# Performance work log

Measured on AMD Instinct MI355X. Metric: run time of the kernel, lower is better.

## Reference

```python
import jax, jax.numpy as jnp
import numpy as np

NUM_HEADS = 16
HEAD_DIM = 32  # out_ch 512 / 16 heads

def _c(x):
    # last axis holds (real, imag) -> complex64
    return jax.lax.complex(x[..., 0], x[..., 1])

def setup_inputs() -> dict:
    key = jax.random.key(0)
    ks = jax.random.split(key, 9)
    B, S, C = 1, 2048, 512
    mk = lambda k, shp: jax.random.normal(k, shp, dtype=jnp.float32)
    return {
        "Q": mk(ks[0], (B, S, C, 2)),
        "V": mk(ks[1], (B, S, C, 2)),
        "K": mk(ks[2], (B, S, C, 2)),
        "Wq": mk(ks[3], (C, C, 2)) * (1.0 / np.sqrt(C)),
        "bq": mk(ks[4], (C, 2)) * 0.02,
        "Wk": mk(ks[5], (C, C, 2)) * (1.0 / np.sqrt(C)),
        "bk": mk(ks[6], (C, 2)) * 0.02,
        "Wv": mk(ks[7], (C, C, 2)) * (1.0 / np.sqrt(C)),
        "bv": mk(ks[8], (C, 2)) * 0.02,
    }

def _split_heads(x):
    B, S, D = x.shape
    return x.reshape(B, S, NUM_HEADS, HEAD_DIM).transpose(0, 2, 1, 3)  # [B,H,S,d]

def reference(Q, V, K, Wq, bq, Wk, bk, Wv, bv):
    Qc, Kc, Vc = _c(Q), _c(K), _c(V)
    # torch Linear: y = x @ W^T + b, W is [out, in]
    proj = lambda x, W, b: jnp.einsum('bsi,oi->bso', x, _c(W)) + _c(b)
    q = _split_heads(proj(Qc, Wq, bq))  # [B,H,S,d] complex64
    k = _split_heads(proj(Kc, Wk, bk))
    v = _split_heads(proj(Vc, Wv, bv))
    scores = jnp.einsum('bhqd,bhkd->bhqk', q, jnp.conj(k)) / np.sqrt(HEAD_DIM).astype(np.float32)
    weights = jax.nn.softmax(jnp.abs(scores), axis=-1)  # real [B,H,S,S]
    out = jnp.einsum('bhqk,bhkd->bhqd', weights.astype(v.dtype), v)  # complex
    B, H, S, d = out.shape
    out = out.transpose(0, 2, 1, 3).reshape(B, S, H * d)  # [B,S,out_ch]
    return jnp.stack([out.real, out.imag], axis=-1)  # [B,S,out_ch,2] float32
```

## Files before the change

kernel.cpp:

```cpp
#include <hip/hip_runtime.h>
#include <hip/hip_bf16.h>
#include <math.h>

#define S_LEN 2048
#define C_DIM 512
#define NH 16
#define HD 32
#define PLANE_U (NH * S_LEN * HD)
#define XF_OFF  (6*(size_t)PLANE_U)
#define WF_OFF  (12*(size_t)PLANE_U)
#define WPLF 262144

typedef __attribute__((ext_vector_type(8)))  short bf16x8;
typedef __attribute__((ext_vector_type(4)))  float f32x4;
typedef __attribute__((ext_vector_type(16))) float f32x16;
typedef __attribute__((ext_vector_type(4)))  unsigned int u32x4;

#if __has_builtin(__builtin_amdgcn_exp2f)
#define EXP2(x) __builtin_amdgcn_exp2f(x)
#else
#define EXP2(x) exp2f(x)
#endif

__device__ __forceinline__ unsigned int pk_bf16(float a, float b) {
    float2 f; f.x = a; f.y = b;
    __hip_bfloat162 t = __float22bfloat162_rn(f);
    return *reinterpret_cast<unsigned int*>(&t);
}

__global__ __launch_bounds__(256)
void xwcvt(const float* __restrict__ Q, const float* __restrict__ K,
           const float* __restrict__ V,
           const float* __restrict__ Wq, const float* __restrict__ Wk,
           const float* __restrict__ Wv, unsigned short* __restrict__ ws)
{
    if (blockIdx.x < 1536) {
        const int tid  = blockIdx.x*256 + threadIdx.x;
        const int z    = tid >> 17;
        const int rem  = tid & 131071;
        const int kidx = rem >> 11;
        const int s    = rem & 2047;
        const int k    = kidx * 8;
        const float2* x2 = (const float2*)(z == 0 ? Q : (z == 1 ? K : V));
        const float4* s4 = (const float4*)(x2 + (size_t)s*C_DIM + k);
        float4 f0 = s4[0], f1 = s4[1], f2v = s4[2], f3 = s4[3];
        u32x4 rh, ih;
        rh[0] = pk_bf16(f0.x, f0.z); rh[1] = pk_bf16(f1.x, f1.z);
        rh[2] = pk_bf16(f2v.x, f2v.z); rh[3] = pk_bf16(f3.x, f3.z);
        ih[0] = pk_bf16(f0.y, f0.w); ih[1] = pk_bf16(f1.y, f1.w);
        ih[2] = pk_bf16(f2v.y, f2v.w); ih[3] = pk_bf16(f3.y, f3.w);
        const int sb = s >> 4, lr = s & 15, g = kidx & 3, kc = kidx >> 2;
        const size_t off = ((size_t)(sb*16 + kc)*64 + g*16 + lr)*8;
        unsigned short* base = ws + XF_OFF + (size_t)z*2*PLANE_U;
        *(u32x4*)&base[off]           = rh;
        *(u32x4*)&base[PLANE_U + off] = ih;
    } else {
        const int tid  = (blockIdx.x - 1536)*256 + threadIdx.x;
        const int z    = tid >> 15;
        const int rem  = tid & 32767;
        const int kidx = rem >> 9;
        const int o    = rem & 511;
        const int k    = kidx * 8;
        const float2* w2 = (const float2*)(z == 0 ? Wq : (z == 1 ? Wk : Wv));
        const float4* s4 = (const float4*)(w2 + (size_t)o*C_DIM + k);
        float4 f0 = s4[0], f1 = s4[1], f2v = s4[2], f3 = s4[3];
        u32x4 rh, ih;
        rh[0] = pk_bf16(f0.x, f0.z); rh[1] = pk_bf16(f1.x, f1.z);
        rh[2] = pk_bf16(f2v.x, f2v.z); rh[3] = pk_bf16(f3.x, f3.z);
        ih[0] = pk_bf16(f0.y, f0.w); ih[1] = pk_bf16(f1.y, f1.w);
        ih[2] = pk_bf16(f2v.y, f2v.w); ih[3] = pk_bf16(f3.y, f3.w);
        const int ob = o >> 4, lr = o & 15, g = kidx & 3, kc = kidx >> 2;
        const size_t off = ((size_t)(ob*16 + kc)*64 + g*16 + lr)*8;
        unsigned short* base = ws + WF_OFF + (size_t)z*2*WPLF;
        *(u32x4*)&base[off]        = rh;
        *(u32x4*)&base[WPLF + off] = ih;
    }
}

__global__ __launch_bounds__(256)
void proj_mfma(const float* __restrict__ bq, const float* __restrict__ bk,
               const float* __restrict__ bv,
               unsigned short* __restrict__ ws)
{
    const int z = blockIdx.z;
    const float* b = (z == 0) ? bq : (z == 1 ? bk : bv);

    const int s0 = blockIdx.x * 32;
    const int o0 = blockIdx.y * 64;

    const unsigned short* xfR = ws + XF_OFF + (size_t)z*2*PLANE_U;
    const unsigned short* xfI = xfR + PLANE_U;
    const unsigned short* wfR = ws + WF_OFF + (size_t)z*2*WPLF;
    const unsigned short* wfI = wfR + WPLF;

    const int t    = threadIdx.x;
    const int wave = t >> 6;
    const int lane = t & 63;
    const int lr   = t & 15;
    const int g    = (t & 63) >> 4;

    const int ob = (o0 >> 4) + wave;
    const int sb = s0 >> 4;

    const f32x4 zf = {0.f,0.f,0.f,0.f};
    f32x4 accR[2], accI[2];
    #pragma unroll
    for (int i = 0; i < 2; ++i) { accR[i] = zf; accI[i] = zf; }

    size_t aoff = ((size_t)(ob*16)*64 + lane)*8;
    bf16x8 aRH = *(const bf16x8*)&wfR[aoff];
    bf16x8 aIH = *(const bf16x8*)&wfI[aoff];

    #pragma unroll
    for (int kc = 0; kc < 16; ++kc) {
        bf16x8 aIHn;
        #pragma unroll
        for (int j = 0; j < 4; ++j)
            ((unsigned int*)&aIHn)[j] = ((const unsigned int*)&aIH)[j] ^ 0x80008000u;

        const size_t b0 = ((size_t)(sb*16 + kc)*64 + lane)*8;
        const size_t b1 = ((size_t)((sb+1)*16 + kc)*64 + lane)*8;
        bf16x8 bRH0 = *(const bf16x8*)&xfR[b0];
        bf16x8 bIH0 = *(const bf16x8*)&xfI[b0];
        bf16x8 bRH1 = *(const bf16x8*)&xfR[b1];
        bf16x8 bIH1 = *(const bf16x8*)&xfI[b1];

        bf16x8 aRHc = aRH, aIHc = aIH;
        if (kc < 15) {
            const size_t an = ((size_t)(ob*16 + kc + 1)*64 + lane)*8;
            aRH = *(const bf16x8*)&wfR[an];
            aIH = *(const bf16x8*)&wfI[an];
        }

        accR[0] = __builtin_amdgcn_mfma_f32_16x16x32_bf16(aRHc, bRH0, accR[0], 0,0,0);
        accR[0] = __builtin_amdgcn_mfma_f32_16x16x32_bf16(aIHn, bIH0, accR[0], 0,0,0);
        accI[0] = __builtin_amdgcn_mfma_f32_16x16x32_bf16(aRHc, bIH0, accI[0], 0,0,0);
        accI[0] = __builtin_amdgcn_mfma_f32_16x16x32_bf16(aIHc, bRH0, accI[0], 0,0,0);
        accR[1] = __builtin_amdgcn_mfma_f32_16x16x32_bf16(aRHc, bRH1, accR[1], 0,0,0);
        accR[1] = __builtin_amdgcn_mfma_f32_16x16x32_bf16(aIHn, bIH1, accR[1], 0,0,0);
        accI[1] = __builtin_amdgcn_mfma_f32_16x16x32_bf16(aRHc, bIH1, accI[1], 0,0,0);
        accI[1] = __builtin_amdgcn_mfma_f32_16x16x32_bf16(aIHc, bRH1, accI[1], 0,0,0);
    }

    const float2* b2 = (const float2*)b;
    const int obase = o0 + wave*16 + g*4;
    const int hh = obase >> 5, d0 = obase & 31;
    float bR[4], bI[4];
    #pragma unroll
    for (int r = 0; r < 4; ++r) { float2 bb = b2[obase + r]; bR[r] = bb.x; bI[r] = bb.y; }

    if (z == 0) {
        const float osc = 0.2550348677f;
        unsigned short* pr = ws;
        unsigned short* pi = pr + PLANE_U;
        #pragma unroll
        for (int tile = 0; tile < 2; ++tile) {
            int s = s0 + tile*16 + lr;
            size_t idx = ((size_t)hh*S_LEN + s)*HD + d0;
            uint2 pkR, pkI;
            pkR.x = pk_bf16((accR[tile][0]+bR[0])*osc, (accR[tile][1]+bR[1])*osc);
            pkR.y = pk_bf16((accR[tile][2]+bR[2])*osc, (accR[tile][3]+bR[3])*osc);
            pkI.x = pk_bf16((accI[tile][0]+bI[0])*osc, (accI[tile][1]+bI[1])*osc);
            pkI.y = pk_bf16((accI[tile][2]+bI[2])*osc, (accI[tile][3]+bI[3])*osc);
            *(uint2*)&pr[idx] = pkR;
            *(uint2*)&pi[idx] = pkI;
        }
    } else if (z == 1) {
        unsigned short* kf = ws + 2*(size_t)PLANE_U;
        const int frag_re = (d0 >= 16) ? 1 : 0;
        const int bsel    = (d0 & 15) >> 3;
        const int e       = d0 & 7;
        #pragma unroll
        for (int tile = 0; tile < 2; ++tile) {
            int s = s0 + tile*16 + lr;
            int c = s >> 5;
            int i = s & 31;
            int r = (i & ~12) | ((i & 4) << 1) | ((i & 8) >> 1);
            int lane2 = bsel*32 + r;
            size_t base = ((size_t)(hh*64 + c)*4)*512 + lane2*8 + e;
            uint2 pkR, pkI;
            pkR.x = pk_bf16(accR[tile][0]+bR[0], accR[tile][1]+bR[1]);
            pkR.y = pk_bf16(accR[tile][2]+bR[2], accR[tile][3]+bR[3]);
            pkI.x = pk_bf16(accI[tile][0]+bI[0], accI[tile][1]+bI[1]);
            pkI.y = pk_bf16(accI[tile][2]+bI[2], accI[tile][3]+bI[3]);
            *(uint2*)&kf[base + (size_t)frag_re*512]     = pkR;
            *(uint2*)&kf[base + (size_t)(2+frag_re)*512] = pkI;
        }
    } else {
        unsigned short* vf = ws + 4*(size_t)PLANE_U;
        const int bsel = lr >> 3;
        const int e    = lr & 7;
        #pragma unroll
        for (int tile = 0; tile < 2; ++tile) {
            int s = s0 + tile*16 + lr;
            const int c       = s >> 5;
            const int frag_re = (s & 31) >= 16 ? 1 : 0;
            const size_t cb   = ((size_t)(hh*64 + c)*4)*512;
            #pragma unroll
            for (int r = 0; r < 4; ++r) {
                int lane2 = bsel*32 + d0 + r;
                size_t base = cb + (size_t)lane2*8 + e;
                vf[base + (size_t)frag_re*512]     =
                    (unsigned short)pk_bf16(accR[tile][r]+bR[r], 0.f);
                vf[base + (size_t)(2+frag_re)*512] =
                    (unsigned short)pk_bf16(accI[tile][r]+bI[r], 0.f);
            }
        }
    }
}

#define RROW 33

__global__ __launch_bounds__(256, 4)
void attn_mfma(const unsigned short* __restrict__ ws, float* __restrict__ out)
{
    const int bid   = blockIdx.x;
    const int h     = bid & (NH - 1);
    const int qblk  = bid >> 4;
    const int wave  = threadIdx.x >> 6;
    const int l     = threadIdx.x & 63;
    const int q     = l & 31;
    const int b     = l >> 5;

    const unsigned short* qr = ws + 0*(size_t)PLANE_U + (size_t)h*S_LEN*HD;
    const unsigned short* qi = ws + 1*(size_t)PLANE_U + (size_t)h*S_LEN*HD;
    const unsigned short* kf = ws + 2*(size_t)PLANE_U + ((size_t)h << 17);
    const unsigned short* vf = ws + 4*(size_t)PLANE_U + ((size_t)h << 17);

    const int q0 = qblk * 32;

    bf16x8 bQr_lo = *(const bf16x8*)&qr[(size_t)(q0 + q)*HD + b*8];
    bf16x8 bQr_hi = *(const bf16x8*)&qr[(size_t)(q0 + q)*HD + 16 + b*8];
    bf16x8 bQi_lo = *(const bf16x8*)&qi[(size_t)(q0 + q)*HD + b*8];
    bf16x8 bQi_hi = *(const bf16x8*)&qi[(size_t)(q0 + q)*HD + 16 + b*8];

    __shared__ __align__(16) float2 red[2*32*RROW];

    f32x16 accR, accI;
    #pragma unroll
    for (int r = 0; r < 16; ++r) { accR[r] = 0.f; accI[r] = 0.f; }
    float lsum = 0.f;

    const f32x16 z16 = {0,0,0,0,0,0,0,0,0,0,0,0,0,0,0,0};
    const int kbeg = wave * 512;
    for (int k0 = kbeg; k0 < kbeg + 512; k0 += 32) {
        const size_t fb = (size_t)(k0 >> 5) * 2048 + l*8;

        bf16x8 aVr_lo = *(const bf16x8*)&vf[fb];
        bf16x8 aVr_hi = *(const bf16x8*)&vf[fb + 512];
        bf16x8 aVi_lo = *(const bf16x8*)&vf[fb + 1024];
        bf16x8 aVi_hi = *(const bf16x8*)&vf[fb + 1536];

        bf16x8 aKr_lo = *(const bf16x8*)&kf[fb];
        bf16x8 aKr_hi = *(const bf16x8*)&kf[fb + 512];
        bf16x8 aKi_lo = *(const bf16x8*)&kf[fb + 1024];
        bf16x8 aKi_hi = *(const bf16x8*)&kf[fb + 1536];
        bf16x8 aKin_lo, aKin_hi;
        #pragma unroll
        for (int j = 0; j < 4; ++j) {
            ((unsigned int*)&aKin_lo)[j] = ((const unsigned int*)&aKi_lo)[j] ^ 0x80008000u;
            ((unsigned int*)&aKin_hi)[j] = ((const unsigned int*)&aKi_hi)[j] ^ 0x80008000u;
        }
        __builtin_amdgcn_s_setprio(1);
        f32x16 sR = __builtin_amdgcn_mfma_f32_32x32x16_bf16(aKr_lo,  bQr_lo, z16, 0, 0, 0);
        f32x16 sI = __builtin_amdgcn_mfma_f32_32x32x16_bf16(aKin_lo, bQr_lo, z16, 0, 0, 0);
        sR = __builtin_amdgcn_mfma_f32_32x32x16_bf16(aKr_hi,  bQr_hi, sR, 0, 0, 0);
        sI = __builtin_amdgcn_mfma_f32_32x32x16_bf16(aKin_hi, bQr_hi, sI, 0, 0, 0);
        sR = __builtin_amdgcn_mfma_f32_32x32x16_bf16(aKi_lo,  bQi_lo, sR, 0, 0, 0);
        sI = __builtin_amdgcn_mfma_f32_32x32x16_bf16(aKr_lo,  bQi_lo, sI, 0, 0, 0);
        sR = __builtin_amdgcn_mfma_f32_32x32x16_bf16(aKi_hi,  bQi_hi, sR, 0, 0, 0);
        sI = __builtin_amdgcn_mfma_f32_32x32x16_bf16(aKr_hi,  bQi_hi, sI, 0, 0, 0);
        __builtin_amdgcn_s_setprio(0);

        bf16x8 bP1, bP2;
        unsigned int* p1 = (unsigned int*)&bP1;
        unsigned int* p2 = (unsigned int*)&bP2;
        #pragma unroll
        for (int r2 = 0; r2 < 8; ++r2) {
            int r = 2*r2;
            float v0 = EXP2(__builtin_amdgcn_sqrtf(fmaf(sR[r],   sR[r],   sI[r]*sI[r])));
            float v1 = EXP2(__builtin_amdgcn_sqrtf(fmaf(sR[r+1], sR[r+1], sI[r+1]*sI[r+1])));
            lsum += v0 + v1;
            if (r2 < 4) p1[r2]     = pk_bf16(v0, v1);
            else        p2[r2 - 4] = pk_bf16(v0, v1);
        }
        __builtin_amdgcn_s_setprio(1);
        accR = __builtin_amdgcn_mfma_f32_32x32x16_bf16(aVr_lo, bP1, accR, 0, 0, 0);
        accI = __builtin_amdgcn_mfma_f32_32x32x16_bf16(aVi_lo, bP1, accI, 0, 0, 0);
        accR = __builtin_amdgcn_mfma_f32_32x32x16_bf16(aVr_hi, bP2, accR, 0, 0, 0);
        accI = __builtin_amdgcn_mfma_f32_32x32x16_bf16(aVi_hi, bP2, accI, 0, 0, 0);
        __builtin_amdgcn_s_setprio(0);
    }

    lsum += __shfl_xor(lsum, 32);

    const int rrow = ((wave & 1) * 32 + q) * RROW;
    __syncthreads();
    if (wave < 2) {
        #pragma unroll
        for (int r = 0; r < 16; ++r) {
            int d = (r & 3) + 8*(r >> 2) + 4*b;
            red[rrow + d] = make_float2(accR[r], accI[r]);
        }
        if (b == 0) red[rrow + 32].x = lsum;
    }
    __syncthreads();
    if (wave >= 2) {
        #pragma unroll
        for (int r = 0; r < 16; ++r) {
            int d = (r & 3) + 8*(r >> 2) + 4*b;
            float2 v = red[rrow + d];
            v.x += accR[r]; v.y += accI[r];
            red[rrow + d] = v;
        }
        if (b == 0) red[rrow + 32].x += lsum;
    }
    __syncthreads();

    {
        const int i  = threadIdx.x;
        const int oq = i >> 3;
        const int d0 = (i & 7) * 4;
        float sl = red[oq*RROW + 32].x + red[(32 + oq)*RROW + 32].x;
        float inv = 1.0f / sl;
        float2* o2 = (float2*)out;
        #pragma unroll
        for (int dd = 0; dd < 4; ++dd) {
            int d = d0 + dd;
            float2 v0 = red[oq*RROW + d];
            float2 v1 = red[(32 + oq)*RROW + d];
            o2[(size_t)(q0 + oq)*C_DIM + h*HD + d] =
                make_float2((v0.x + v1.x)*inv, (v0.y + v1.y)*inv);
        }
    }
}

extern "C" void kernel_launch(void* const* d_in, const int* in_sizes, int n_in,
                              void* d_out, int out_size, void* d_ws, size_t ws_size,
                              hipStream_t stream)
{
    const float* Q  = (const float*)d_in[0];
    const float* V  = (const float*)d_in[1];
    const float* K  = (const float*)d_in[2];
    const float* Wq = (const float*)d_in[3];
    const float* bq = (const float*)d_in[4];
    const float* Wk = (const float*)d_in[5];
    const float* bk = (const float*)d_in[6];
    const float* Wv = (const float*)d_in[7];
    const float* bv = (const float*)d_in[8];
    unsigned short* ws = (unsigned short*)d_ws;
    float* out = (float*)d_out;

    xwcvt<<<1920, 256, 0, stream>>>(Q, K, V, Wq, Wk, Wv, ws);
    proj_mfma<<<dim3(S_LEN/32, C_DIM/64, 3), 256, 0, stream>>>(bq, bk, bv, ws);
    attn_mfma<<<dim3(64*NH), 256, 0, stream>>>(ws, out);
}
```

Before: 72.84 us.

## Process two 32-query strips per attention block to reuse K/V fragments

Each attention block now handles 64 queries (two 32-row strips) instead of 32, so every K and V fragment loaded from global memory feeds twice as many MFMA score and PV products. The grid is halved to 512 blocks and the launch-bounds occupancy hint is dropped to allow the higher register use of four accumulators. The cross-wave reduction and output write are looped over the two strips. The aim is to cut K/V load traffic per FLOP, at the cost of more VGPRs, lower occupancy and fewer blocks to spread across the CUs.

```diff
diff --git a/kernel.cpp b/kernel.cpp
--- a/kernel.cpp
+++ b/kernel.cpp
@@ -211,7 +211,7 @@
 
 #define RROW 33
 
-__global__ __launch_bounds__(256, 4)
+__global__ __launch_bounds__(256)
 void attn_mfma(const unsigned short* __restrict__ ws, float* __restrict__ out)
 {
     const int bid   = blockIdx.x;
@@ -227,19 +227,26 @@
     const unsigned short* kf = ws + 2*(size_t)PLANE_U + ((size_t)h << 17);
     const unsigned short* vf = ws + 4*(size_t)PLANE_U + ((size_t)h << 17);
 
-    const int q0 = qblk * 32;
-
-    bf16x8 bQr_lo = *(const bf16x8*)&qr[(size_t)(q0 + q)*HD + b*8];
-    bf16x8 bQr_hi = *(const bf16x8*)&qr[(size_t)(q0 + q)*HD + 16 + b*8];
-    bf16x8 bQi_lo = *(const bf16x8*)&qi[(size_t)(q0 + q)*HD + b*8];
-    bf16x8 bQi_hi = *(const bf16x8*)&qi[(size_t)(q0 + q)*HD + 16 + b*8];
+    const int q0 = qblk * 64;
+
+    bf16x8 bQr_loA = *(const bf16x8*)&qr[(size_t)(q0 + q)*HD + b*8];
+    bf16x8 bQr_hiA = *(const bf16x8*)&qr[(size_t)(q0 + q)*HD + 16 + b*8];
+    bf16x8 bQi_loA = *(const bf16x8*)&qi[(size_t)(q0 + q)*HD + b*8];
+    bf16x8 bQi_hiA = *(const bf16x8*)&qi[(size_t)(q0 + q)*HD + 16 + b*8];
+    bf16x8 bQr_loB = *(const bf16x8*)&qr[(size_t)(q0 + 32 + q)*HD + b*8];
+    bf16x8 bQr_hiB = *(const bf16x8*)&qr[(size_t)(q0 + 32 + q)*HD + 16 + b*8];
+    bf16x8 bQi_loB = *(const bf16x8*)&qi[(size_t)(q0 + 32 + q)*HD + b*8];
+    bf16x8 bQi_hiB = *(const bf16x8*)&qi[(size_t)(q0 + 32 + q)*HD + 16 + b*8];
 
     __shared__ __align__(16) float2 red[2*32*RROW];
 
-    f32x16 accR, accI;
-    #pragma unroll
-    for (int r = 0; r < 16; ++r) { accR[r] = 0.f; accI[r] = 0.f; }
-    float lsum = 0.f;
+    f32x16 accRA, accIA, accRB, accIB;
+    #pragma unroll
+    for (int r = 0; r < 16; ++r) {
+        accRA[r] = 0.f; accIA[r] = 0.f;
+        accRB[r] = 0.f; accIB[r] = 0.f;
+    }
+    float lsumA = 0.f, lsumB = 0.f;
 
     const f32x16 z16 = {0,0,0,0,0,0,0,0,0,0,0,0,0,0,0,0};
     const int kbeg = wave * 512;
@@ -261,75 +268,109 @@
             ((unsigned int*)&aKin_lo)[j] = ((const unsigned int*)&aKi_lo)[j] ^ 0x80008000u;
             ((unsigned int*)&aKin_hi)[j] = ((const unsigned int*)&aKi_hi)[j] ^ 0x80008000u;
         }
+
+        bf16x8 bP1A, bP2A, bP1B, bP2B;
+        {
+            __builtin_amdgcn_s_setprio(1);
+            f32x16 sR = __builtin_amdgcn_mfma_f32_32x32x16_bf16(aKr_lo,  bQr_loA, z16, 0, 0, 0);
+            f32x16 sI = __builtin_amdgcn_mfma_f32_32x32x16_bf16(aKin_lo, bQr_loA, z16, 0, 0, 0);
+            sR = __builtin_amdgcn_mfma_f32_32x32x16_bf16(aKr_hi,  bQr_hiA, sR, 0, 0, 0);
+            sI = __builtin_amdgcn_mfma_f32_32x32x16_bf16(aKin_hi, bQr_hiA, sI, 0, 0, 0);
+            sR = __builtin_amdgcn_mfma_f32_32x32x16_bf16(aKi_lo,  bQi_loA, sR, 0, 0, 0);
+            sI = __builtin_amdgcn_mfma_f32_32x32x16_bf16(aKr_lo,  bQi_loA, sI, 0, 0, 0);
+            sR = __builtin_amdgcn_mfma_f32_32x32x16_bf16(aKi_hi,  bQi_hiA, sR, 0, 0, 0);
+            sI = __builtin_amdgcn_mfma_f32_32x32x16_bf16(aKr_hi,  bQi_hiA, sI, 0, 0, 0);
+            __builtin_amdgcn_s_setprio(0);
+            unsigned int* p1 = (unsigned int*)&bP1A;
+            unsigned int* p2 = (unsigned int*)&bP2A;
+            #pragma unroll
+            for (int r2 = 0; r2 < 8; ++r2) {
+                int r = 2*r2;
+                float v0 = EXP2(__builtin_amdgcn_sqrtf(fmaf(sR[r],   sR[r],   sI[r]*sI[r])));
+                float v1 = EXP2(__builtin_amdgcn_sqrtf(fmaf(sR[r+1], sR[r+1], sI[r+1]*sI[r+1])));
+                lsumA += v0 + v1;
+                if (r2 < 4) p1[r2]     = pk_bf16(v0, v1);
+                else        p2[r2 - 4] = pk_bf16(v0, v1);
+            }
+        }
+        {
+            __builtin_amdgcn_s_setprio(1);
+            f32x16 sR = __builtin_amdgcn_mfma_f32_32x32x16_bf16(aKr_lo,  bQr_loB, z16, 0, 0, 0);
+            f32x16 sI = __builtin_amdgcn_mfma_f32_32x32x16_bf16(aKin_lo, bQr_loB, z16, 0, 0, 0);
+            sR = __builtin_amdgcn_mfma_f32_32x32x16_bf16(aKr_hi,  bQr_hiB, sR, 0, 0, 0);
+            sI = __builtin_amdgcn_mfma_f32_32x32x16_bf16(aKin_hi, bQr_hiB, sI, 0, 0, 0);
+            sR = __builtin_amdgcn_mfma_f32_32x32x16_bf16(aKi_lo,  bQi_loB, sR, 0, 0, 0);
+            sI = __builtin_amdgcn_mfma_f32_32x32x16_bf16(aKr_lo,  bQi_loB, sI, 0, 0, 0);
+            sR = __builtin_amdgcn_mfma_f32_32x32x16_bf16(aKi_hi,  bQi_hiB, sR, 0, 0, 0);
+            sI = __builtin_amdgcn_mfma_f32_32x32x16_bf16(aKr_hi,  bQi_hiB, sI, 0, 0, 0);
+            __builtin_amdgcn_s_setprio(0);
+            unsigned int* p1 = (unsigned int*)&bP1B;
+            unsigned int* p2 = (unsigned int*)&bP2B;
+            #pragma unroll
+            for (int r2 = 0; r2 < 8; ++r2) {
+                int r = 2*r2;
+                float v0 = EXP2(__builtin_amdgcn_sqrtf(fmaf(sR[r],   sR[r],   sI[r]*sI[r])));
+                float v1 = EXP2(__builtin_amdgcn_sqrtf(fmaf(sR[r+1], sR[r+1], sI[r+1]*sI[r+1])));
+                lsumB += v0 + v1;
+                if (r2 < 4) p1[r2]     = pk_bf16(v0, v1);
+                else        p2[r2 - 4] = pk_bf16(v0, v1);
+            }
+        }
         __builtin_amdgcn_s_setprio(1);
-        f32x16 sR = __builtin_amdgcn_mfma_f32_32x32x16_bf16(aKr_lo,  bQr_lo, z16, 0, 0, 0);
-        f32x16 sI = __builtin_amdgcn_mfma_f32_32x32x16_bf16(aKin_lo, bQr_lo, z16, 0, 0, 0);
-        sR = __builtin_amdgcn_mfma_f32_32x32x16_bf16(aKr_hi,  bQr_hi, sR, 0, 0, 0);
-        sI = __builtin_amdgcn_mfma_f32_32x32x16_bf16(aKin_hi, bQr_hi, sI, 0, 0, 0);
-        sR = __builtin_amdgcn_mfma_f32_32x32x16_bf16(aKi_lo,  bQi_lo, sR, 0, 0, 0);
-        sI = __builtin_amdgcn_mfma_f32_32x32x16_bf16(aKr_lo,  bQi_lo, sI, 0, 0, 0);
-        sR = __builtin_amdgcn_mfma_f32_32x32x16_bf16(aKi_hi,  bQi_hi, sR, 0, 0, 0);
-        sI = __builtin_amdgcn_mfma_f32_32x32x16_bf16(aKr_hi,  bQi_hi, sI, 0, 0, 0);
+        accRA = __builtin_amdgcn_mfma_f32_32x32x16_bf16(aVr_lo, bP1A, accRA, 0, 0, 0);
+        accIA = __builtin_amdgcn_mfma_f32_32x32x16_bf16(aVi_lo, bP1A, accIA, 0, 0, 0);
+        accRB = __builtin_amdgcn_mfma_f32_32x32x16_bf16(aVr_lo, bP1B, accRB, 0, 0, 0);
+        accIB = __builtin_amdgcn_mfma_f32_32x32x16_bf16(aVi_lo, bP1B, accIB, 0, 0, 0);
+        accRA = __builtin_amdgcn_mfma_f32_32x32x16_bf16(aVr_hi, bP2A, accRA, 0, 0, 0);
+        accIA = __builtin_amdgcn_mfma_f32_32x32x16_bf16(aVi_hi, bP2A, accIA, 0, 0, 0);
+        accRB = __builtin_amdgcn_mfma_f32_32x32x16_bf16(aVr_hi, bP2B, accRB, 0, 0, 0);
+        accIB = __builtin_amdgcn_mfma_f32_32x32x16_bf16(aVi_hi, bP2B, accIB, 0, 0, 0);
         __builtin_amdgcn_s_setprio(0);
-
-        bf16x8 bP1, bP2;
-        unsigned int* p1 = (unsigned int*)&bP1;
-        unsigned int* p2 = (unsigned int*)&bP2;
-        #pragma unroll
-        for (int r2 = 0; r2 < 8; ++r2) {
-            int r = 2*r2;
-            float v0 = EXP2(__builtin_amdgcn_sqrtf(fmaf(sR[r],   sR[r],   sI[r]*sI[r])));
-            float v1 = EXP2(__builtin_amdgcn_sqrtf(fmaf(sR[r+1], sR[r+1], sI[r+1]*sI[r+1])));
-            lsum += v0 + v1;
-            if (r2 < 4) p1[r2]     = pk_bf16(v0, v1);
-            else        p2[r2 - 4] = pk_bf16(v0, v1);
-        }
-        __builtin_amdgcn_s_setprio(1);
-        accR = __builtin_amdgcn_mfma_f32_32x32x16_bf16(aVr_lo, bP1, accR, 0, 0, 0);
-        accI = __builtin_amdgcn_mfma_f32_32x32x16_bf16(aVi_lo, bP1, accI, 0, 0, 0);
-        accR = __builtin_amdgcn_mfma_f32_32x32x16_bf16(aVr_hi, bP2, accR, 0, 0, 0);
-        accI = __builtin_amdgcn_mfma_f32_32x32x16_bf16(aVi_hi, bP2, accI, 0, 0, 0);
-        __builtin_amdgcn_s_setprio(0);
-    }
-
-    lsum += __shfl_xor(lsum, 32);
+    }
+
+    lsumA += __shfl_xor(lsumA, 32);
+    lsumB += __shfl_xor(lsumB, 32);
 
     const int rrow = ((wave & 1) * 32 + q) * RROW;
-    __syncthreads();
-    if (wave < 2) {
-        #pragma unroll
-        for (int r = 0; r < 16; ++r) {
-            int d = (r & 3) + 8*(r >> 2) + 4*b;
-            red[rrow + d] = make_float2(accR[r], accI[r]);
-        }
-        if (b == 0) red[rrow + 32].x = lsum;
-    }
-    __syncthreads();
-    if (wave >= 2) {
-        #pragma unroll
-        for (int r = 0; r < 16; ++r) {
-            int d = (r & 3) + 8*(r >> 2) + 4*b;
-            float2 v = red[rrow + d];
-            v.x += accR[r]; v.y += accI[r];
-            red[rrow + d] = v;
-        }
-        if (b == 0) red[rrow + 32].x += lsum;
-    }
-    __syncthreads();
-
-    {
+    float2* o2 = (float2*)out;
+    #pragma unroll
+    for (int strip = 0; strip < 2; ++strip) {
+        const f32x16& cR = strip ? accRB : accRA;
+        const f32x16& cI = strip ? accIB : accIA;
+        const float   lv = strip ? lsumB : lsumA;
+        const int  qbase = q0 + strip*32;
+        __syncthreads();
+        if (wave < 2) {
+            #pragma unroll
+            for (int r = 0; r < 16; ++r) {
+                int d = (r & 3) + 8*(r >> 2) + 4*b;
+                red[rrow + d] = make_float2(cR[r], cI[r]);
+            }
+            if (b == 0) red[rrow + 32].x = lv;
+        }
+        __syncthreads();
+        if (wave >= 2) {
+            #pragma unroll
+            for (int r = 0; r < 16; ++r) {
+                int d = (r & 3) + 8*(r >> 2) + 4*b;
+                float2 v = red[rrow + d];
+                v.x += cR[r]; v.y += cI[r];
+                red[rrow + d] = v;
+            }
+            if (b == 0) red[rrow + 32].x += lv;
+        }
+        __syncthreads();
         const int i  = threadIdx.x;
         const int oq = i >> 3;
         const int d0 = (i & 7) * 4;
         float sl = red[oq*RROW + 32].x + red[(32 + oq)*RROW + 32].x;
         float inv = 1.0f / sl;
-        float2* o2 = (float2*)out;
         #pragma unroll
         for (int dd = 0; dd < 4; ++dd) {
             int d = d0 + dd;
             float2 v0 = red[oq*RROW + d];
             float2 v1 = red[(32 + oq)*RROW + d];
-            o2[(size_t)(q0 + oq)*C_DIM + h*HD + d] =
+            o2[(size_t)(qbase + oq)*C_DIM + h*HD + d] =
                 make_float2((v0.x + v1.x)*inv, (v0.y + v1.y)*inv);
         }
     }
@@ -353,5 +394,5 @@
 
     xwcvt<<<1920, 256, 0, stream>>>(Q, K, V, Wq, Wk, Wv, ws);
     proj_mfma<<<dim3(S_LEN/32, C_DIM/64, 3), 256, 0, stream>>>(bq, bk, bv, ws);
-    attn_mfma<<<dim3(64*NH), 256, 0, stream>>>(ws, out);
-}
+    attn_mfma<<<dim3(32*NH), 256, 0, stream>>>(ws, out);
+}
```

Result: slower. 74.86 us (+2.8%).
